# Optimization experiments

Hardware: AMD Instinct MI355X
Metric: run time of the kernel (lower is better)

Reference implementation:

```python
import jax, jax.numpy as jnp
import numpy as np

B, S, H = 8, 512, 768
NH, DH = 12, 64
I = 3072
E = 8
TOPK = 2
EPS = 1e-12


def _ln(x, g, b):
    m = jnp.mean(x, axis=-1, keepdims=True)
    v = jnp.mean(jnp.square(x - m), axis=-1, keepdims=True)
    return (x - m) * jax.lax.rsqrt(v + EPS) * g + b


def setup_inputs() -> dict:
    key = jax.random.key(0)
    ks = jax.random.split(key, 20)
    s_h = 1.0 / np.sqrt(H)
    s_i = 1.0 / np.sqrt(I)
    inp = {
        "hidden_states": jax.random.normal(ks[0], (B, S, H), jnp.float32),
        "Wq": jax.random.normal(ks[1], (H, H), jnp.float32) * s_h,
        "bq": jnp.zeros((H,), jnp.float32),
        "Wk": jax.random.normal(ks[2], (H, H), jnp.float32) * s_h,
        "bk": jnp.zeros((H,), jnp.float32),
        "Wv": jax.random.normal(ks[3], (H, H), jnp.float32) * s_h,
        "bv": jnp.zeros((H,), jnp.float32),
        "Wo": jax.random.normal(ks[4], (H, H), jnp.float32) * s_h,
        "bo": jnp.zeros((H,), jnp.float32),
        "ln_attn_g": jnp.ones((H,), jnp.float32),
        "ln_attn_b": jnp.zeros((H,), jnp.float32),
        "ln_ffn_g": jnp.ones((H,), jnp.float32),
        "ln_ffn_b": jnp.zeros((H,), jnp.float32),
        "Wr": jax.random.normal(ks[5], (H, E), jnp.float32) * s_h,
        "br": jnp.zeros((E,), jnp.float32),
        "W_up": jax.random.normal(ks[6], (E, H, I), jnp.float32) * s_h,
        "b_up": jnp.zeros((E, I), jnp.float32),
        "W_new": jax.random.normal(ks[7], (E, H, I), jnp.float32) * s_h,
        "b_new": jnp.zeros((E, I), jnp.float32),
        "W_down": jax.random.normal(ks[8], (E, I, H), jnp.float32) * s_i,
        "b_down": jnp.zeros((E, H), jnp.float32),
    }
    return inp


def reference(hidden_states, Wq, bq, Wk, bk, Wv, bv, Wo, bo,
              ln_attn_g, ln_attn_b, ln_ffn_g, ln_ffn_b,
              Wr, br, W_up, b_up, W_new, b_new, W_down, b_down):
    x = hidden_states
    # --- BertSelfAttention ---
    q = (x @ Wq + bq).reshape(B, S, NH, DH).transpose(0, 2, 1, 3)
    k = (x @ Wk + bk).reshape(B, S, NH, DH).transpose(0, 2, 1, 3)
    v = (x @ Wv + bv).reshape(B, S, NH, DH).transpose(0, 2, 1, 3)
    scores = jnp.einsum("bhqd,bhkd->bhqk", q, k) / np.sqrt(DH)
    probs = jax.nn.softmax(scores, axis=-1)
    ctx = jnp.einsum("bhqk,bhkd->bhqd", probs, v)
    ctx = ctx.transpose(0, 2, 1, 3).reshape(B, S, H)
    # --- BertSelfOutput: dense + residual + LayerNorm ---
    attention_output = _ln(ctx @ Wo + bo + x, ln_attn_g, ln_attn_b)
    # --- feed_forward_chunk: LayerNorm then token top-k MoE ---
    xl = _ln(attention_output, ln_ffn_g, ln_ffn_b)
    router_logits = xl @ Wr + br                      # [B,S,E]
    router_probs = jax.nn.softmax(router_logits, axis=-1)
    topw, topi = jax.lax.top_k(router_probs, TOPK)    # [B,S,K]
    topw = topw / jnp.sum(topw, axis=-1, keepdims=True)
    gates = jnp.sum(jax.nn.one_hot(topi, E, dtype=xl.dtype) * topw[..., None], axis=-2)  # [B,S,E]
    # --- experts (BertExpert: gelu(up(x)) * new(x) -> down), dense over E ---
    up = jax.nn.gelu(jnp.einsum("bsh,ehi->ebsi", xl, W_up) + b_up[:, None, None, :], approximate=False)
    gate_h = jnp.einsum("bsh,ehi->ebsi", xl, W_new) + b_new[:, None, None, :]
    y = jnp.einsum("ebsi,eih->ebsh", up * gate_h, W_down) + b_down[:, None, None, :]
    moe_out = jnp.einsum("ebsh,bse->bsh", y, gates)
    layer_output = moe_out + attention_output
    return layer_output, router_logits
```

## Files before the change

kernel.cpp:

```cpp
#include <hip/hip_runtime.h>
#include <hip/hip_bf16.h>
#include <cmath>


constexpr int cB = 8, cS = 512, cH = 768, cNH = 12, cDH = 64, cI = 3072, cE = 8;
constexpr int cT = cB * cS;
constexpr size_t TH = (size_t)cT * cH;

typedef __hip_bfloat16 bf16;
typedef __attribute__((ext_vector_type(8))) short s8v;
typedef __attribute__((ext_vector_type(4))) float f4v;

constexpr size_t SZ_WEXP     = (size_t)cE * cI * cH / 2;
constexpr size_t OFF_WUP_T   = 0;
constexpr size_t OFF_WNEW_T  = OFF_WUP_T + SZ_WEXP;
constexpr size_t OFF_WDOWN_T = OFF_WNEW_T + SZ_WEXP;
constexpr size_t OFF_QKV     = OFF_WDOWN_T + SZ_WEXP;
constexpr size_t OFF_CTX     = OFF_QKV + 4 * TH;
constexpr size_t OFF_XLB     = OFF_CTX + TH;
constexpr size_t OFF_WGT     = OFF_XLB + TH / 2;
constexpr size_t OFF_COUNTS  = OFF_WGT + 2 * cT;
constexpr size_t OFF_LISTS   = OFF_COUNTS + 16;

__device__ __forceinline__ void glds16(const void* g, void* l) {
    __builtin_amdgcn_global_load_lds(
        (const __attribute__((address_space(1))) unsigned int*)g,
        (__attribute__((address_space(3))) unsigned int*)l, 16, 0, 0);
}

__global__ void init_counts_kernel(int* __restrict__ counts) {
    if (threadIdx.x < cE) counts[threadIdx.x] = 0;
}

__global__ __launch_bounds__(256) void transpose_bf16_kernel(
    const float* __restrict__ src, bf16* __restrict__ dst, int R, int C) {
    __shared__ float tile[64][65];
    const size_t zb = (size_t)blockIdx.z * R * C;
    const int r0 = blockIdx.y * 64, c0 = blockIdx.x * 64;
    const int t = threadIdx.x;
    const int lr = t >> 4, lc = (t & 15) * 4;
#pragma unroll
    for (int i = 0; i < 4; ++i) {
        float4 v = *(const float4*)(src + zb + (size_t)(r0 + lr + i * 16) * C + c0 + lc);
        tile[lr + i * 16][lc + 0] = v.x; tile[lr + i * 16][lc + 1] = v.y;
        tile[lr + i * 16][lc + 2] = v.z; tile[lr + i * 16][lc + 3] = v.w;
    }
    __syncthreads();
#pragma unroll
    for (int i = 0; i < 4; ++i) {
        int cr = lr + i * 16;
        bf16 o[4];
#pragma unroll
        for (int j = 0; j < 4; ++j) o[j] = (bf16)tile[lc + j][cr];
        *(uint2*)(dst + zb + (size_t)(c0 + cr) * R + r0 + lc) = *(uint2*)o;
    }
}

__device__ __forceinline__ void gemm_body_sg(
    const float* __restrict__ A, const float* __restrict__ B,
    const float* __restrict__ bias, float* __restrict__ C,
    int N, int K, int m0, int n0, int kbeg, int kend, bool addb) {
    __shared__ float Bs[16 * 256];
    const int t = threadIdx.x;
    const int wv = t >> 6, l = t & 63;
    const int wu = __builtin_amdgcn_readfirstlane(wv);
    const float* Ab = A + (size_t)(m0 + wu * 8) * K;
    const float* gB = B + (size_t)(kbeg + wv * 4) * N + n0 + l * 4;
    float* dB = Bs + (wv * 4) * 256 + l * 4;
    float acc[8][4] = {};
    for (int k0 = kbeg; k0 < kend; k0 += 16) {
        glds16(gB, dB);
        glds16(gB + (size_t)N, dB + 256);
        glds16(gB + (size_t)2 * N, dB + 512);
        glds16(gB + (size_t)3 * N, dB + 768);
        __syncthreads();
#pragma unroll
        for (int q = 0; q < 4; ++q) {
            float4 a4[8];
#pragma unroll
            for (int r = 0; r < 8; ++r)
                a4[r] = *(const float4*)(Ab + (size_t)r * K + k0 + q * 4);
#pragma unroll
            for (int kq = 0; kq < 4; ++kq) {
                float4 b = *(const float4*)&Bs[(q * 4 + kq) * 256 + l * 4];
#pragma unroll
                for (int r = 0; r < 8; ++r) {
                    float av = (kq == 0) ? a4[r].x : (kq == 1) ? a4[r].y
                             : (kq == 2) ? a4[r].z : a4[r].w;
                    acc[r][0] += av * b.x;
                    acc[r][1] += av * b.y;
                    acc[r][2] += av * b.z;
                    acc[r][3] += av * b.w;
                }
            }
        }
        __syncthreads();
        gB += (size_t)16 * N;
    }
#pragma unroll
    for (int r = 0; r < 8; ++r) {
        int m = m0 + wu * 8 + r;
        float4 o;
        o.x = acc[r][0]; o.y = acc[r][1]; o.z = acc[r][2]; o.w = acc[r][3];
        if (addb) {
            o.x += bias[n0 + l * 4 + 0];
            o.y += bias[n0 + l * 4 + 1];
            o.z += bias[n0 + l * 4 + 2];
            o.w += bias[n0 + l * 4 + 3];
        }
        *(float4*)(C + (size_t)m * N + n0 + l * 4) = o;
    }
}

__global__ __launch_bounds__(256) void gemm_qkv_kernel(
    const float* __restrict__ A,
    const float* __restrict__ Wq, const float* __restrict__ Wk,
    const float* __restrict__ Wv,
    const float* __restrict__ bq, const float* __restrict__ bk,
    const float* __restrict__ bv,
    float* __restrict__ q0, float* __restrict__ k0, float* __restrict__ v0,
    float* __restrict__ q1, float* __restrict__ k1, float* __restrict__ v1) {
    const int f = blockIdx.x + 3 * blockIdx.y + 384 * blockIdx.z;
    const int xcd = f & 7, p = f >> 3;
    const int yl = p & 15;
    const int n  = (p >> 4) % 3;
    const int pz = p / 48;
    const int y  = xcd * 16 + yl;
    const int proj = pz >> 1, ks = pz & 1;
    const float* B = (proj == 0) ? Wq : (proj == 1) ? Wk : Wv;
    const float* bias = (proj == 0) ? bq : (proj == 1) ? bk : bv;
    float* C = (proj == 0) ? (ks ? q1 : q0)
             : (proj == 1) ? (ks ? k1 : k0)
                           : (ks ? v1 : v0);
    gemm_body_sg(A, B, bias, C, cH, cH, y * 32, n * 256,
                 ks * 384, ks * 384 + 384, ks == 0);
}

__global__ __launch_bounds__(256) void reduce_qkv_kernel(
    float* __restrict__ dst2, const float* __restrict__ src2,
    float* __restrict__ v0, const float* __restrict__ v1) {
    const size_t n2 = 2 * TH / 4, n3 = 3 * TH / 4;
    for (size_t i = (size_t)blockIdx.x * 256 + threadIdx.x; i < n3;
         i += (size_t)gridDim.x * 256) {
        if (i < n2) {
            float4 a = ((const float4*)dst2)[i];
            float4 b = ((const float4*)src2)[i];
            a.x += b.x; a.y += b.y; a.z += b.z; a.w += b.w;
            ((float4*)dst2)[i] = a;
        } else {
            size_t j = i - n2;
            float4 a = ((const float4*)v0)[j];
            float4 b = ((const float4*)v1)[j];
            a.x += b.x; a.y += b.y; a.z += b.z; a.w += b.w;
            ((float4*)v0)[j] = a;
        }
    }
}

__global__ __launch_bounds__(256) void gemm_wo_kernel(
    const float* __restrict__ A, const float* __restrict__ W,
    const float* __restrict__ bias,
    float* __restrict__ p0, float* __restrict__ p1,
    float* __restrict__ p2, float* __restrict__ p3) {
    const int f = blockIdx.x + 3 * blockIdx.y + 384 * blockIdx.z;
    const int xcd = f & 7, p = f >> 3;
    const int yl = p & 15;
    const int n  = (p >> 4) % 3;
    const int ks = p / 48;
    const int y  = xcd * 16 + yl;
    float* C = (ks == 0) ? p0 : (ks == 1) ? p1 : (ks == 2) ? p2 : p3;
    gemm_body_sg(A, W, bias, C, cH, cH, y * 32, n * 256,
                 ks * 192, ks * 192 + 192, ks == 0);
}

__global__ __launch_bounds__(256) void attn_kernel(
    const float* __restrict__ q, const float* __restrict__ k,
    const float* __restrict__ v, float* __restrict__ ctx) {
    __shared__ float sQ[64][68];
    __shared__ float sKV[64][68];
    __shared__ float sS[64][68];
    __shared__ float sM[64], sL[64], sAl[64];
    const int q0 = blockIdx.x * 64, h = blockIdx.y, b = blockIdx.z;
    const int t = threadIdx.x;
    const int lr = t >> 2, lq = (t & 3) * 16;
    {
        const float* gq = q + (size_t)(b * cS + q0 + lr) * cH + h * cDH + lq;
#pragma unroll
        for (int j = 0; j < 4; ++j) {
            float4 x = *(const float4*)(gq + j * 4);
            x.x *= 0.125f; x.y *= 0.125f; x.z *= 0.125f; x.w *= 0.125f;
            *(float4*)&sQ[lr][lq + j * 4] = x;
        }
    }
    if (t < 64) { sM[t] = -1e30f; sL[t] = 0.f; }
    const int c0 = t & 15, rr = (t >> 4) * 4;
    const int d4 = (t & 15) * 4, rp = (t >> 4) * 4;
    const int sr = t >> 2, sc = (t & 3) * 16;
    float4 o_acc[4];
#pragma unroll
    for (int i = 0; i < 4; ++i) o_acc[i] = make_float4(0.f, 0.f, 0.f, 0.f);

    for (int kt = 0; kt < 8; ++kt) {
        float4 kreg[4];
        {
            const float* gk = k + (size_t)(b * cS + kt * 64 + lr) * cH + h * cDH + lq;
#pragma unroll
            for (int j = 0; j < 4; ++j) kreg[j] = *(const float4*)(gk + j * 4);
        }
        __syncthreads();
#pragma unroll
        for (int j = 0; j < 4; ++j) *(float4*)&sKV[lr][lq + j * 4] = kreg[j];
        __syncthreads();
        float accS[4][4] = {};
#pragma unroll
        for (int d = 0; d < 64; d += 4) {
            float4 qv[4], kv[4];
#pragma unroll
            for (int i = 0; i < 4; ++i) qv[i] = *(const float4*)&sQ[rr + i][d];
#pragma unroll
            for (int j = 0; j < 4; ++j) kv[j] = *(const float4*)&sKV[c0 + 16 * j][d];
#pragma unroll
            for (int i = 0; i < 4; ++i)
#pragma unroll
                for (int j = 0; j < 4; ++j)
                    accS[i][j] += qv[i].x * kv[j].x + qv[i].y * kv[j].y +
                                  qv[i].z * kv[j].z + qv[i].w * kv[j].w;
        }
#pragma unroll
        for (int i = 0; i < 4; ++i)
#pragma unroll
            for (int j = 0; j < 4; ++j) sS[rr + i][c0 + 16 * j] = accS[i][j];
        float4 vreg[4];
        {
            const float* gv = v + (size_t)(b * cS + kt * 64 + lr) * cH + h * cDH + lq;
#pragma unroll
            for (int j = 0; j < 4; ++j) vreg[j] = *(const float4*)(gv + j * 4);
        }
        __syncthreads();
        {
            float4 s[4];
#pragma unroll
            for (int j = 0; j < 4; ++j) s[j] = *(const float4*)&sS[sr][sc + j * 4];
            float m = -1e30f;
#pragma unroll
            for (int j = 0; j < 4; ++j)
                m = fmaxf(m, fmaxf(fmaxf(s[j].x, s[j].y), fmaxf(s[j].z, s[j].w)));
            m = fmaxf(m, __shfl_xor(m, 1));
            m = fmaxf(m, __shfl_xor(m, 2));
            float m_old = sM[sr];
            float m_new = fmaxf(m_old, m);
            float sum = 0.f;
#pragma unroll
            for (int j = 0; j < 4; ++j) {
                s[j].x = __expf(s[j].x - m_new); s[j].y = __expf(s[j].y - m_new);
                s[j].z = __expf(s[j].z - m_new); s[j].w = __expf(s[j].w - m_new);
                sum += s[j].x + s[j].y + s[j].z + s[j].w;
                *(float4*)&sS[sr][sc + j * 4] = s[j];
            }
            sum += __shfl_xor(sum, 1);
            sum += __shfl_xor(sum, 2);
            if ((t & 3) == 0) {
                float alpha = __expf(m_old - m_new);
                sAl[sr] = alpha;
                sM[sr] = m_new;
                sL[sr] = sL[sr] * alpha + sum;
            }
        }
#pragma unroll
        for (int j = 0; j < 4; ++j) *(float4*)&sKV[lr][lq + j * 4] = vreg[j];
        __syncthreads();
#pragma unroll
        for (int i = 0; i < 4; ++i) {
            float al = sAl[rp + i];
            o_acc[i].x *= al; o_acc[i].y *= al; o_acc[i].z *= al; o_acc[i].w *= al;
        }
        for (int kk4 = 0; kk4 < 64; kk4 += 4) {
            float4 pv[4], vv[4];
#pragma unroll
            for (int i = 0; i < 4; ++i) pv[i] = *(const float4*)&sS[rp + i][kk4];
#pragma unroll
            for (int j = 0; j < 4; ++j) vv[j] = *(const float4*)&sKV[kk4 + j][d4];
#pragma unroll
            for (int i = 0; i < 4; ++i) {
                o_acc[i].x += pv[i].x * vv[0].x + pv[i].y * vv[1].x +
                              pv[i].z * vv[2].x + pv[i].w * vv[3].x;
                o_acc[i].y += pv[i].x * vv[0].y + pv[i].y * vv[1].y +
                              pv[i].z * vv[2].y + pv[i].w * vv[3].y;
                o_acc[i].z += pv[i].x * vv[0].z + pv[i].y * vv[1].z +
                              pv[i].z * vv[2].z + pv[i].w * vv[3].z;
                o_acc[i].w += pv[i].x * vv[0].w + pv[i].y * vv[1].w +
                              pv[i].z * vv[2].w + pv[i].w * vv[3].w;
            }
        }
    }
    __syncthreads();
#pragma unroll
    for (int i = 0; i < 4; ++i) {
        float inv = 1.0f / sL[rp + i];
        float4 o = o_acc[i];
        o.x *= inv; o.y *= inv; o.z *= inv; o.w *= inv;
        *(float4*)(ctx + (size_t)(b * cS + q0 + rp + i) * cH + h * cDH + d4) = o;
    }
}

__device__ __forceinline__ float block_reduce_sum(float v, float* red) {
#pragma unroll
    for (int o = 32; o; o >>= 1) v += __shfl_xor(v, o);
    __syncthreads();
    if ((threadIdx.x & 63) == 0) red[threadIdx.x >> 6] = v;
    __syncthreads();
    return red[0] + red[1] + red[2] + red[3];
}

__global__ __launch_bounds__(256) void ln_router_kernel(
    const float* __restrict__ dense0, const float* __restrict__ dense1,
    const float* __restrict__ dense2, const float* __restrict__ dense3,
    const float* __restrict__ resid,
    const float* __restrict__ g1, const float* __restrict__ b1,
    const float* __restrict__ g2, const float* __restrict__ b2,
    const float* __restrict__ Wr, const float* __restrict__ br,
    float* __restrict__ out, bf16* __restrict__ xlb,
    float* __restrict__ out_logits, float* __restrict__ wgt,
    int* __restrict__ counts, int* __restrict__ lists) {
    __shared__ float red[4];
    __shared__ float lred[4][8];
    const int t = blockIdx.x, tid = threadIdx.x;
    const size_t base = (size_t)t * cH;
    float v[3], s = 0.f;
#pragma unroll
    for (int i = 0; i < 3; ++i) {
        size_t ix = base + tid + 256 * i;
        v[i] = dense0[ix] + dense1[ix] + dense2[ix] + dense3[ix] + resid[ix];
        s += v[i];
    }
    const float mean = block_reduce_sum(s, red) * (1.0f / cH);
    float vs = 0.f;
#pragma unroll
    for (int i = 0; i < 3; ++i) { float d = v[i] - mean; vs += d * d; }
    const float rstd = rsqrtf(block_reduce_sum(vs, red) * (1.0f / cH) + 1e-12f);
    float a[3], s2 = 0.f;
#pragma unroll
    for (int i = 0; i < 3; ++i) {
        a[i] = (v[i] - mean) * rstd * g1[tid + 256 * i] + b1[tid + 256 * i];
        out[base + tid + 256 * i] = a[i];
        s2 += a[i];
    }
    const float mean2 = block_reduce_sum(s2, red) * (1.0f / cH);
    float vs2 = 0.f;
#pragma unroll
    for (int i = 0; i < 3; ++i) { float d = a[i] - mean2; vs2 += d * d; }
    const float rstd2 = rsqrtf(block_reduce_sum(vs2, red) * (1.0f / cH) + 1e-12f);
    float xl[3];
#pragma unroll
    for (int i = 0; i < 3; ++i) {
        xl[i] = (a[i] - mean2) * rstd2 * g2[tid + 256 * i] + b2[tid + 256 * i];
        xlb[base + tid + 256 * i] = (bf16)xl[i];
    }
    float lg[cE] = {};
#pragma unroll
    for (int i = 0; i < 3; ++i) {
        const float* wr = Wr + (size_t)(tid + 256 * i) * cE;
#pragma unroll
        for (int e = 0; e < cE; ++e) lg[e] += xl[i] * wr[e];
    }
#pragma unroll
    for (int e = 0; e < cE; ++e)
#pragma unroll
        for (int o = 32; o; o >>= 1) lg[e] += __shfl_xor(lg[e], o);
    if ((tid & 63) == 0)
#pragma unroll
        for (int e = 0; e < cE; ++e) lred[tid >> 6][e] = lg[e];
    __syncthreads();
    if (tid == 0) {
        float logits[cE];
#pragma unroll
        for (int e = 0; e < cE; ++e) {
            logits[e] = lred[0][e] + lred[1][e] + lred[2][e] + lred[3][e] + br[e];
            out_logits[(size_t)t * cE + e] = logits[e];
        }
        int i0 = 0;
        for (int e = 1; e < cE; ++e) if (logits[e] > logits[i0]) i0 = e;
        int i1 = (i0 == 0) ? 1 : 0;
        for (int e = 0; e < cE; ++e)
            if (e != i0 && logits[e] > logits[i1]) i1 = e;
        float e1 = __expf(logits[i1] - logits[i0]);
        float w0 = 1.0f / (1.0f + e1);
        float w1 = e1 * w0;
        wgt[t * 2 + 0] = w0;
        wgt[t * 2 + 1] = w1;
        int p0 = atomicAdd(&counts[i0], 1);
        lists[i0 * cT + p0] = t * 2 + 0;
        int p1 = atomicAdd(&counts[i1], 1);
        lists[i1 * cT + p1] = t * 2 + 1;
    }
}

__global__ __launch_bounds__(256) void expert_up_mfma_kernel(
    const bf16* __restrict__ xlb,
    const bf16* __restrict__ WupT, const bf16* __restrict__ WnewT,
    const float* __restrict__ b_up, const float* __restrict__ b_new,
    const int* __restrict__ counts, const int* __restrict__ lists,
    bf16* __restrict__ act) {
    const int e = blockIdx.z;
    const int cnt = counts[e];
    const int m0 = blockIdx.y * 128;
    if (m0 >= cnt) return;
    const int n0 = blockIdx.x * 64;
    __shared__ short sA[2 * 128 * 32], sB1[2 * 64 * 32], sB2[2 * 64 * 32];
    __shared__ int rowa[128];
    const int t = threadIdx.x;
    if (t < 128) {
        int idx = m0 + t;
        rowa[t] = (idx < cnt) ? lists[e * cT + idx] : -1;
    }
    __syncthreads();
    const int lane = t & 63, w = t >> 6;
    const int wm = (w >> 1) * 64, wn = (w & 1) * 32;
    const int rA0 = t >> 2, kc8 = (t & 3) * 8;
    int a0 = rowa[rA0], a1 = rowa[rA0 + 64];
    const bf16* gA0 = xlb + (size_t)(a0 < 0 ? 0 : (a0 >> 1)) * cH + kc8;
    const bf16* gA1 = xlb + (size_t)(a1 < 0 ? 0 : (a1 >> 1)) * cH + kc8;
    const bf16* B1 = WupT + (size_t)e * cI * cH;
    const bf16* B2 = WnewT + (size_t)e * cI * cH;
    const bf16* gB1 = B1 + (size_t)(n0 + rA0) * cH + kc8;
    const bf16* gB2 = B2 + (size_t)(n0 + rA0) * cH + kc8;
    short* dA0 = sA + t * 8;
    short* dA1 = sA + (t + 256) * 8;
    short* dA2 = sA + (t + 512) * 8;
    short* dA3 = sA + (t + 768) * 8;
    short* dB1a = sB1 + t * 8;
    short* dB1b = sB1 + (t + 256) * 8;
    short* dB2a = sB2 + t * 8;
    short* dB2b = sB2 + (t + 256) * 8;
    f4v zero = {0.f, 0.f, 0.f, 0.f};
    f4v acc1[4][2], acc2[4][2];
#pragma unroll
    for (int i = 0; i < 4; ++i)
#pragma unroll
        for (int j = 0; j < 2; ++j) { acc1[i][j] = zero; acc2[i][j] = zero; }
    const int fr = lane & 15, kg = (lane >> 4) * 8;
    for (int kk = 0; kk < cH; kk += 64) {
        glds16(gA0 + kk, dA0);      glds16(gA1 + kk, dA1);
        glds16(gA0 + kk + 32, dA2); glds16(gA1 + kk + 32, dA3);
        glds16(gB1 + kk, dB1a);     glds16(gB1 + kk + 32, dB1b);
        glds16(gB2 + kk, dB2a);     glds16(gB2 + kk + 32, dB2b);
        __syncthreads();
#pragma unroll
        for (int ks = 0; ks < 2; ++ks) {
            const short* pA  = sA  + ks * 4096;
            const short* pB1 = sB1 + ks * 2048;
            const short* pB2 = sB2 + ks * 2048;
            s8v af[4], bf1[2], bf2[2];
#pragma unroll
            for (int i = 0; i < 4; ++i)
                af[i] = *(const s8v*)(pA + (wm + i * 16 + fr) * 32 + kg);
#pragma unroll
            for (int j = 0; j < 2; ++j) {
                bf1[j] = *(const s8v*)(pB1 + (wn + j * 16 + fr) * 32 + kg);
                bf2[j] = *(const s8v*)(pB2 + (wn + j * 16 + fr) * 32 + kg);
            }
#pragma unroll
            for (int mi = 0; mi < 4; ++mi)
#pragma unroll
                for (int ni = 0; ni < 2; ++ni) {
                    acc1[mi][ni] = __builtin_amdgcn_mfma_f32_16x16x32_bf16(
                        af[mi], bf1[ni], acc1[mi][ni], 0, 0, 0);
                    acc2[mi][ni] = __builtin_amdgcn_mfma_f32_16x16x32_bf16(
                        af[mi], bf2[ni], acc2[mi][ni], 0, 0, 0);
                }
        }
        __syncthreads();
    }
    const int cn = lane & 15, rq = (lane >> 4) * 4;
#pragma unroll
    for (int mi = 0; mi < 4; ++mi)
#pragma unroll
        for (int r = 0; r < 4; ++r) {
            int ml = wm + mi * 16 + rq + r;
            int a = rowa[ml];
            if (a < 0) continue;
            bf16* orow = act + (size_t)a * cI + n0 + wn;
#pragma unroll
            for (int ni = 0; ni < 2; ++ni) {
                int nl = ni * 16 + cn;
                float up = acc1[mi][ni][r] + b_up[e * cI + n0 + wn + nl];
                float nw = acc2[mi][ni][r] + b_new[e * cI + n0 + wn + nl];
                float g = 0.5f * up * (1.0f + erff(up * 0.70710678118654752f));
                orow[nl] = (bf16)(g * nw);
            }
        }
}

__global__ __launch_bounds__(256) void expert_down_mfma_kernel(
    const bf16* __restrict__ act, const bf16* __restrict__ WdownT,
    const float* __restrict__ b_down,
    const int* __restrict__ counts, const int* __restrict__ lists,
    const float* __restrict__ wgt, float* __restrict__ out) {
    const int e = blockIdx.z;
    const int cnt = counts[e];
    const int m0 = blockIdx.y * 128;
    if (m0 >= cnt) return;
    const int n0 = blockIdx.x * 128;
    __shared__ short sA[2 * 128 * 32], sB[2 * 128 * 32];
    __shared__ int rowa[128];
    const int t = threadIdx.x;
    if (t < 128) {
        int idx = m0 + t;
        rowa[t] = (idx < cnt) ? lists[e * cT + idx] : -1;
    }
    __syncthreads();
    const int lane = t & 63, w = t >> 6;
    const int wm = (w >> 1) * 64, wn = (w & 1) * 64;
    const int rA0 = t >> 2, kc8 = (t & 3) * 8;
    int a0 = rowa[rA0], a1 = rowa[rA0 + 64];
    const bf16* gA0 = act + (size_t)(a0 < 0 ? 0 : a0) * cI + kc8;
    const bf16* gA1 = act + (size_t)(a1 < 0 ? 0 : a1) * cI + kc8;
    const bf16* BT = WdownT + (size_t)e * cH * cI;
    const bf16* gB0 = BT + (size_t)(n0 + rA0) * cI + kc8;
    const bf16* gB1 = BT + (size_t)(n0 + rA0 + 64) * cI + kc8;
    short* dA0 = sA + t * 8;
    short* dA1 = sA + (t + 256) * 8;
    short* dA2 = sA + (t + 512) * 8;
    short* dA3 = sA + (t + 768) * 8;
    short* dB0 = sB + t * 8;
    short* dB1d = sB + (t + 256) * 8;
    short* dB2 = sB + (t + 512) * 8;
    short* dB3 = sB + (t + 768) * 8;
    f4v zero = {0.f, 0.f, 0.f, 0.f};
    f4v acc[4][4];
#pragma unroll
    for (int i = 0; i < 4; ++i)
#pragma unroll
        for (int j = 0; j < 4; ++j) acc[i][j] = zero;
    const int fr = lane & 15, kg = (lane >> 4) * 8;
    for (int kk = 0; kk < cI; kk += 64) {
        glds16(gA0 + kk, dA0);      glds16(gA1 + kk, dA1);
        glds16(gA0 + kk + 32, dA2); glds16(gA1 + kk + 32, dA3);
        glds16(gB0 + kk, dB0);      glds16(gB1 + kk, dB1d);
        glds16(gB0 + kk + 32, dB2); glds16(gB1 + kk + 32, dB3);
        __syncthreads();
#pragma unroll
        for (int ks = 0; ks < 2; ++ks) {
            const short* pA = sA + ks * 4096;
            const short* pB = sB + ks * 4096;
            s8v af[4], bf[4];
#pragma unroll
            for (int i = 0; i < 4; ++i)
                af[i] = *(const s8v*)(pA + (wm + i * 16 + fr) * 32 + kg);
#pragma unroll
            for (int i = 0; i < 4; ++i)
                bf[i] = *(const s8v*)(pB + (wn + i * 16 + fr) * 32 + kg);
#pragma unroll
            for (int mi = 0; mi < 4; ++mi)
#pragma unroll
                for (int ni = 0; ni < 4; ++ni)
                    acc[mi][ni] = __builtin_amdgcn_mfma_f32_16x16x32_bf16(
                        af[mi], bf[ni], acc[mi][ni], 0, 0, 0);
        }
        __syncthreads();
    }
    const int cn = lane & 15, rq = (lane >> 4) * 4;
#pragma unroll
    for (int mi = 0; mi < 4; ++mi)
#pragma unroll
        for (int r = 0; r < 4; ++r) {
            int ml = wm + mi * 16 + rq + r;
            int a = rowa[ml];
            if (a < 0) continue;
            int token = a >> 1;
            float wv = wgt[a];
#pragma unroll
            for (int ni = 0; ni < 4; ++ni) {
                int n = n0 + wn + ni * 16 + cn;
                atomicAdd(&out[(size_t)token * cH + n],
                          wv * (acc[mi][ni][r] + b_down[e * cH + n]));
            }
        }
}

extern "C" void kernel_launch(void* const* d_in, const int* in_sizes, int n_in,
                              void* d_out, int out_size, void* d_ws, size_t ws_size,
                              hipStream_t stream) {
    const float* x      = (const float*)d_in[0];
    const float* Wq     = (const float*)d_in[1];
    const float* bq     = (const float*)d_in[2];
    const float* Wk     = (const float*)d_in[3];
    const float* bk     = (const float*)d_in[4];
    const float* Wv     = (const float*)d_in[5];
    const float* bv     = (const float*)d_in[6];
    const float* Wo     = (const float*)d_in[7];
    const float* bo     = (const float*)d_in[8];
    const float* ln1g   = (const float*)d_in[9];
    const float* ln1b   = (const float*)d_in[10];
    const float* ln2g   = (const float*)d_in[11];
    const float* ln2b   = (const float*)d_in[12];
    const float* Wr     = (const float*)d_in[13];
    const float* br     = (const float*)d_in[14];
    const float* W_up   = (const float*)d_in[15];
    const float* b_up   = (const float*)d_in[16];
    const float* W_new  = (const float*)d_in[17];
    const float* b_new  = (const float*)d_in[18];
    const float* W_down = (const float*)d_in[19];
    const float* b_down = (const float*)d_in[20];

    float* out = (float*)d_out;
    float* ws  = (float*)d_ws;

    bf16* WupT   = (bf16*)(ws + OFF_WUP_T);
    bf16* WnewT  = (bf16*)(ws + OFF_WNEW_T);
    bf16* WdownT = (bf16*)(ws + OFF_WDOWN_T);
    float* q     = ws + OFF_QKV;
    float* k     = ws + OFF_QKV + TH;
    float* v     = ws + OFF_QKV + 2 * TH;
    float* tmp   = ws + OFF_QKV + 3 * TH;
    bf16* act    = (bf16*)(ws + OFF_QKV);
    float* ctx   = ws + OFF_CTX;
    bf16* xlb    = (bf16*)(ws + OFF_XLB);
    float* wgt   = ws + OFF_WGT;
    int* counts  = (int*)(ws + OFF_COUNTS);
    int* lists   = (int*)(ws + OFF_LISTS);

    init_counts_kernel<<<1, 64, 0, stream>>>(counts);

    transpose_bf16_kernel<<<dim3(48, 12, cE), 256, 0, stream>>>(W_up, WupT, cH, cI);
    transpose_bf16_kernel<<<dim3(48, 12, cE), 256, 0, stream>>>(W_new, WnewT, cH, cI);
    transpose_bf16_kernel<<<dim3(12, 48, cE), 256, 0, stream>>>(W_down, WdownT, cI, cH);

    gemm_qkv_kernel<<<dim3(3, 128, 6), 256, 0, stream>>>(
        x, Wq, Wk, Wv, bq, bk, bv, q, k, v, tmp, ctx, out);
    reduce_qkv_kernel<<<2048, 256, 0, stream>>>(q, tmp, v, out);
    attn_kernel<<<dim3(cS / 64, cNH, cB), 256, 0, stream>>>(q, k, v, ctx);
    gemm_wo_kernel<<<dim3(3, 128, 4), 256, 0, stream>>>(
        ctx, Wo, bo, q, k, v, tmp);
    ln_router_kernel<<<cT, 256, 0, stream>>>(
        q, k, v, tmp, x, ln1g, ln1b, ln2g, ln2b, Wr, br,
        out, xlb, out + TH, wgt, counts, lists);

    expert_up_mfma_kernel<<<dim3(cI / 64, cT / 128, cE), 256, 0, stream>>>(
        xlb, WupT, WnewT, b_up, b_new, counts, lists, act);
    expert_down_mfma_kernel<<<dim3(cH / 128, cT / 128, cE), 256, 0, stream>>>(
        act, WdownT, b_down, counts, lists, wgt, out);
}
```

Measured before the change: 1.025 ms.

## Double-buffer LDS tiles in expert MFMA GEMMs to overlap loads with compute

Both expert GEMM kernels now use two LDS buffers. The next K-tile is prefetched with direct global-to-LDS loads while MFMAs run on the current tile, which removes one barrier per iteration and hides global load latency behind compute. In exchange, LDS use per block doubles (about 64KB for the down kernel), which can lower occupancy. Correctness also depends on the end-of-loop barrier, together with the asynchronous load completion, ordering each prefetch before its buffer is consumed.

```diff
diff --git a/kernel.cpp b/kernel.cpp
--- a/kernel.cpp
+++ b/kernel.cpp
@@ -406,7 +406,7 @@
     const int m0 = blockIdx.y * 128;
     if (m0 >= cnt) return;
     const int n0 = blockIdx.x * 64;
-    __shared__ short sA[2 * 128 * 32], sB1[2 * 64 * 32], sB2[2 * 64 * 32];
+    __shared__ short sA[2][8192], sB1[2][4096], sB2[2][4096];
     __shared__ int rowa[128];
     const int t = threadIdx.x;
     if (t < 128) {
@@ -424,14 +424,16 @@
     const bf16* B2 = WnewT + (size_t)e * cI * cH;
     const bf16* gB1 = B1 + (size_t)(n0 + rA0) * cH + kc8;
     const bf16* gB2 = B2 + (size_t)(n0 + rA0) * cH + kc8;
-    short* dA0 = sA + t * 8;
-    short* dA1 = sA + (t + 256) * 8;
-    short* dA2 = sA + (t + 512) * 8;
-    short* dA3 = sA + (t + 768) * 8;
-    short* dB1a = sB1 + t * 8;
-    short* dB1b = sB1 + (t + 256) * 8;
-    short* dB2a = sB2 + t * 8;
-    short* dB2b = sB2 + (t + 256) * 8;
+    auto stage = [&](int bi, int kk) {
+        glds16(gA0 + kk,      &sA[bi][t * 8]);
+        glds16(gA1 + kk,      &sA[bi][(t + 256) * 8]);
+        glds16(gA0 + kk + 32, &sA[bi][(t + 512) * 8]);
+        glds16(gA1 + kk + 32, &sA[bi][(t + 768) * 8]);
+        glds16(gB1 + kk,      &sB1[bi][t * 8]);
+        glds16(gB1 + kk + 32, &sB1[bi][(t + 256) * 8]);
+        glds16(gB2 + kk,      &sB2[bi][t * 8]);
+        glds16(gB2 + kk + 32, &sB2[bi][(t + 256) * 8]);
+    };
     f4v zero = {0.f, 0.f, 0.f, 0.f};
     f4v acc1[4][2], acc2[4][2];
 #pragma unroll
@@ -439,17 +441,16 @@
 #pragma unroll
         for (int j = 0; j < 2; ++j) { acc1[i][j] = zero; acc2[i][j] = zero; }
     const int fr = lane & 15, kg = (lane >> 4) * 8;
+    stage(0, 0);
+    __syncthreads();
+    int buf = 0;
     for (int kk = 0; kk < cH; kk += 64) {
-        glds16(gA0 + kk, dA0);      glds16(gA1 + kk, dA1);
-        glds16(gA0 + kk + 32, dA2); glds16(gA1 + kk + 32, dA3);
-        glds16(gB1 + kk, dB1a);     glds16(gB1 + kk + 32, dB1b);
-        glds16(gB2 + kk, dB2a);     glds16(gB2 + kk + 32, dB2b);
-        __syncthreads();
+        if (kk + 64 < cH) stage(buf ^ 1, kk + 64);
 #pragma unroll
         for (int ks = 0; ks < 2; ++ks) {
-            const short* pA  = sA  + ks * 4096;
-            const short* pB1 = sB1 + ks * 2048;
-            const short* pB2 = sB2 + ks * 2048;
+            const short* pA  = &sA[buf][ks * 4096];
+            const short* pB1 = &sB1[buf][ks * 2048];
+            const short* pB2 = &sB2[buf][ks * 2048];
             s8v af[4], bf1[2], bf2[2];
 #pragma unroll
             for (int i = 0; i < 4; ++i)
@@ -470,6 +471,7 @@
                 }
         }
         __syncthreads();
+        buf ^= 1;
     }
     const int cn = lane & 15, rq = (lane >> 4) * 4;
 #pragma unroll
@@ -501,7 +503,7 @@
     const int m0 = blockIdx.y * 128;
     if (m0 >= cnt) return;
     const int n0 = blockIdx.x * 128;
-    __shared__ short sA[2 * 128 * 32], sB[2 * 128 * 32];
+    __shared__ short sA[2][8192], sB[2][8192];
     __shared__ int rowa[128];
     const int t = threadIdx.x;
     if (t < 128) {
@@ -518,14 +520,16 @@
     const bf16* BT = WdownT + (size_t)e * cH * cI;
     const bf16* gB0 = BT + (size_t)(n0 + rA0) * cI + kc8;
     const bf16* gB1 = BT + (size_t)(n0 + rA0 + 64) * cI + kc8;
-    short* dA0 = sA + t * 8;
-    short* dA1 = sA + (t + 256) * 8;
-    short* dA2 = sA + (t + 512) * 8;
-    short* dA3 = sA + (t + 768) * 8;
-    short* dB0 = sB + t * 8;
-    short* dB1d = sB + (t + 256) * 8;
-    short* dB2 = sB + (t + 512) * 8;
-    short* dB3 = sB + (t + 768) * 8;
+    auto stage = [&](int bi, int kk) {
+        glds16(gA0 + kk,      &sA[bi][t * 8]);
+        glds16(gA1 + kk,      &sA[bi][(t + 256) * 8]);
+        glds16(gA0 + kk + 32, &sA[bi][(t + 512) * 8]);
+        glds16(gA1 + kk + 32, &sA[bi][(t + 768) * 8]);
+        glds16(gB0 + kk,      &sB[bi][t * 8]);
+        glds16(gB1 + kk,      &sB[bi][(t + 256) * 8]);
+        glds16(gB0 + kk + 32, &sB[bi][(t + 512) * 8]);
+        glds16(gB1 + kk + 32, &sB[bi][(t + 768) * 8]);
+    };
     f4v zero = {0.f, 0.f, 0.f, 0.f};
     f4v acc[4][4];
 #pragma unroll
@@ -533,16 +537,15 @@
 #pragma unroll
         for (int j = 0; j < 4; ++j) acc[i][j] = zero;
     const int fr = lane & 15, kg = (lane >> 4) * 8;
+    stage(0, 0);
+    __syncthreads();
+    int buf = 0;
     for (int kk = 0; kk < cI; kk += 64) {
-        glds16(gA0 + kk, dA0);      glds16(gA1 + kk, dA1);
-        glds16(gA0 + kk + 32, dA2); glds16(gA1 + kk + 32, dA3);
-        glds16(gB0 + kk, dB0);      glds16(gB1 + kk, dB1d);
-        glds16(gB0 + kk + 32, dB2); glds16(gB1 + kk + 32, dB3);
-        __syncthreads();
+        if (kk + 64 < cI) stage(buf ^ 1, kk + 64);
 #pragma unroll
         for (int ks = 0; ks < 2; ++ks) {
-            const short* pA = sA + ks * 4096;
-            const short* pB = sB + ks * 4096;
+            const short* pA = &sA[buf][ks * 4096];
+            const short* pB = &sB[buf][ks * 4096];
             s8v af[4], bf[4];
 #pragma unroll
             for (int i = 0; i < 4; ++i)
@@ -558,6 +561,7 @@
                         af[mi], bf[ni], acc[mi][ni], 0, 0, 0);
         }
         __syncthreads();
+        buf ^= 1;
     }
     const int cn = lane & 15, rq = (lane >> 4) * 4;
 #pragma unroll
```

Result: no change. 1.024 ms (-0.1%).
